# Optimization experiments

Measured on AMD Instinct MI355X. Metric: run time of the kernel, lower is better.

Reference implementation:

```python
import jax, jax.numpy as jnp
import numpy as np

NOISE_LEVEL = 0.01
MASK_RATIO = 0.3
CG_TOL = 1e-7
CG_MAXITER = 300
# 8-connected neighbor offsets and weights (sum to 1), as in ROAD
OFFSETS = [((1, 1), 1.0 / 12.0), ((0, 1), 1.0 / 6.0), ((-1, 1), 1.0 / 12.0),
           ((1, -1), 1.0 / 12.0), ((0, -1), 1.0 / 6.0), ((-1, -1), 1.0 / 12.0),
           ((1, 0), 1.0 / 6.0), ((-1, 0), 1.0 / 6.0)]


def _shift(f, dy, dx):
    # out[..., r, c] = f[..., r+dy, c+dx], zero outside the grid (invalid neighbors)
    H, W = f.shape[-2], f.shape[-1]
    pad = [(0, 0)] * (f.ndim - 2) + [(1, 1), (1, 1)]
    fp = jnp.pad(f, pad)
    return fp[..., 1 + dy:1 + dy + H, 1 + dx:1 + dx + W]


def _stencil(f):
    # weighted sum over valid 8-neighbors (zero padding encodes validity)
    return sum(w * _shift(f, dy, dx) for (dy, dx), w in OFFSETS)


def _road_mask_morf_by_area(smap, ratio):
    # mask==0 -> pixel is imputed; MoRF masks the top `ratio` fraction by saliency
    B, H, W = smap.shape
    k = int(round(ratio * H * W))
    top_idx = jnp.argsort(-smap.reshape(B, -1), axis=1)[:, :k]  # (B, k)
    mask = jnp.ones((B, H * W), jnp.float32)
    mask = mask.at[jnp.arange(B)[:, None], top_idx].set(0.0)
    return mask.reshape(B, H, W)


def _impute(img, mask, noise):
    # Solves the same sparse linear system as ROAD._setup_sparse_system + spsolve,
    # expressed matrix-free on the pixel grid: for each unknown pixel i,
    #   S_i * x_i - sum_{valid unknown nb j} w_ij x_j = sum_{valid known nb j} w_ij img_j
    # where S_i = sum of valid-neighbor weights (== sum_neighbors in the torch code).
    # This is an SPD graph-Laplacian system; CG converges to the direct-solve answer.
    m = mask[:, None]            # (B,1,H,W); 1 = known pixel
    unk = 1.0 - m                # 1 = unknown pixel
    H, W = img.shape[-2], img.shape[-1]
    S = _stencil(jnp.ones((H, W), img.dtype))    # (H,W) valid-neighbor weight sums
    rhs = unk * _stencil(m * img)                # == -b of the torch assembly

    def Aop(x):
        # identity on known pixels keeps the operator SPD over the full grid
        return jnp.where(unk > 0, S * x - _stencil(unk * x), x)

    x, _ = jax.scipy.sparse.linalg.cg(Aop, rhs, tol=CG_TOL, maxiter=CG_MAXITER)
    return m * img + unk * (x + NOISE_LEVEL * noise)


def setup_inputs() -> dict:
    key = jax.random.key(0)
    k1, k2, k3 = jax.random.split(key, 3)
    B, C, H, W = 16, 3, 512, 512
    img = jax.random.normal(k1, (B, C, H, W), jnp.float32)
    smap = jax.random.randint(k2, (B, H, W), 0, 1000000, jnp.int32)
    noise = jax.random.normal(k3, (B, C, H, W), jnp.float32)
    return {"img": img, "smap": smap, "noise": noise}


def reference(img, smap, noise):
    mask = _road_mask_morf_by_area(smap, MASK_RATIO)   # (B,H,W), 0 = impute
    imputed = _impute(img, mask, noise)                # (B,C,H,W)
    return imputed, mask
```

## Files before the change

### kernel.cpp

```cpp
#include <hip/hip_runtime.h>
#include <cstdint>
#include <cstddef>

#define HW 512
#define SPATIAL (HW*HW)
#define BATCH 16
#define CH 3
#define NPLANE (BATCH*CH)
#define NELEM ((size_t)NPLANE*SPATIAL)
#define GROWS (NPLANE*HW)
#define K_SELECT 78643
#define NITER 8
#define CAP_TIES 4096
#define NSLOT 64
#define PAD 8
#define RBAND 4
#define CBAND 6

typedef _Float16 h16;
typedef __attribute__((ext_vector_type(8))) _Float16 h16x8;
typedef __attribute__((ext_vector_type(8))) float f32x8;

static const size_t OFF_P0   = 0;
static const size_t OFF_P1   = NELEM*2;
static const size_t OFF_P2   = NELEM*4;
static const size_t OFF_BITS = NELEM*6;
static const size_t OFF_X    = OFF_BITS + (size_t)BATCH*8192*4;
static const size_t OFF_DOTS = OFF_X + NELEM*2;
static const size_t OFF_BETA = OFF_DOTS + (size_t)(NITER+1)*3*NSLOT*PAD*8;
static const size_t OFF_ALPH = OFF_BETA + (size_t)(NITER+1)*8;
static const size_t OFF_HC   = OFF_ALPH + (size_t)(NITER+1)*8;
static const size_t OFF_HF   = OFF_HC + (size_t)BATCH*1024*4;
static const size_t OFF_SEL  = OFF_HF + (size_t)BATCH*1024*4;
static const size_t OFF_TC   = OFF_SEL + (size_t)BATCH*4*4;
static const size_t OFF_TL   = OFF_TC + 64;

__global__ __launch_bounds__(256) void k_hist_coarse(const int* __restrict__ smap, int* __restrict__ hist){
  __shared__ int h[1024];
  int tid = threadIdx.x;
  for (int j=tid;j<1024;j+=256) h[j]=0;
  __syncthreads();
  int b = blockIdx.y;
  int base = b*SPATIAL + blockIdx.x*4096;
  #pragma unroll
  for (int e=0;e<16;e++){
    int v = smap[base + e*256 + tid];
    atomicAdd(&h[v>>10], 1);
  }
  __syncthreads();
  for (int j=tid;j<1024;j+=256){ int c=h[j]; if(c) atomicAdd(&hist[b*1024+j], c); }
}

__global__ __launch_bounds__(1024) void k_select_coarse(const int* __restrict__ hist, int* __restrict__ sel){
  int lane = threadIdx.x, b = threadIdx.y;
  const int* h = hist + b*1024;
  int loc[16]; int s=0;
  #pragma unroll
  for (int j=0;j<16;j++){ loc[j]=h[lane*16+j]; s+=loc[j]; }
  int T=s;
  #pragma unroll
  for (int o=1;o<64;o<<=1){ int t=__shfl_down(T,o,64); if (lane+o<64) T+=t; }
  int S = T - s;
  if (S < K_SELECT && T >= K_SELECT){
    int acc=S;
    #pragma unroll
    for (int j=15;j>=0;j--){
      acc+=loc[j];
      if (acc>=K_SELECT){ sel[b*4+0]=lane*16+j; sel[b*4+1]=acc-loc[j]; break; }
    }
  }
}

__global__ __launch_bounds__(256) void k_hist_fine(const int* __restrict__ smap, const int* __restrict__ sel, int* __restrict__ hist){
  __shared__ int h[1024];
  int tid=threadIdx.x;
  for (int j=tid;j<1024;j+=256) h[j]=0;
  __syncthreads();
  int b=blockIdx.y;
  int cb = sel[b*4+0];
  int base = b*SPATIAL + blockIdx.x*4096;
  #pragma unroll
  for (int e=0;e<16;e++){
    int v = smap[base+e*256+tid];
    if ((v>>10)==cb) atomicAdd(&h[v&1023],1);
  }
  __syncthreads();
  for (int j=tid;j<1024;j+=256){ int c=h[j]; if(c) atomicAdd(&hist[b*1024+j],c); }
}

__global__ __launch_bounds__(1024) void k_select_fine(const int* __restrict__ hist, int* __restrict__ sel){
  int lane = threadIdx.x, b = threadIdx.y;
  const int* h = hist + b*1024;
  int cb = sel[b*4+0];
  int acc0 = sel[b*4+1];
  int loc[16]; int s=0;
  #pragma unroll
  for (int j=0;j<16;j++){ loc[j]=h[lane*16+j]; s+=loc[j]; }
  int T=s;
  #pragma unroll
  for (int o=1;o<64;o<<=1){ int t=__shfl_down(T,o,64); if (lane+o<64) T+=t; }
  int S = acc0 + (T - s);
  int Ti = acc0 + T;
  if (S < K_SELECT && Ti >= K_SELECT){
    int acc=S;
    #pragma unroll
    for (int j=15;j>=0;j--){
      acc+=loc[j];
      if (acc>=K_SELECT){
        sel[b*4+2]=(cb<<10)|(lane*16+j);
        sel[b*4+3]=K_SELECT-(acc-loc[j]);
        break;
      }
    }
  }
}

__global__ __launch_bounds__(256) void k_mask_init(const int* __restrict__ smap, const int* __restrict__ sel,
                                                   float* __restrict__ mask, uint32_t* __restrict__ bits,
                                                   int* __restrict__ tiecnt, int* __restrict__ tielist){
  int idx = blockIdx.x*256+threadIdx.x;
  int b = idx>>18;
  int v = smap[idx];
  int T = sel[b*4+2];
  bool unk = (v>T);
  unsigned long long bal = __ballot(unk);
  if ((threadIdx.x&63)==0){
    bits[idx>>5]     = (uint32_t)(bal);
    bits[(idx>>5)+1] = (uint32_t)(bal>>32);
  }
  if (v==T){
    int t = atomicAdd(&tiecnt[b],1);
    if (t<CAP_TIES) tielist[b*CAP_TIES+t] = idx & (SPATIAL-1);
  }
  mask[idx]= unk? 0.f : 1.f;
}

__global__ __launch_bounds__(256) void k_tie_fix(const int* __restrict__ sel, const int* __restrict__ tiecnt,
                                                 const int* __restrict__ tielist, float* __restrict__ mask,
                                                 uint32_t* __restrict__ bits){
  int b=blockIdx.x;
  int n = tiecnt[b]; if (n>CAP_TIES) n=CAP_TIES;
  int need = sel[b*4+3];
  for (int e=threadIdx.x; e<n; e+=256){
    int me = tielist[b*CAP_TIES+e];
    int rank=0;
    for (int j=0;j<n;j++) rank += (tielist[b*CAP_TIES+j] < me) ? 1:0;
    if (rank<need){
      mask[b*SPATIAL+me]=0.f;
      atomicOr(&bits[(b<<13)+(me>>5)], 1u<<(me&31));
    }
  }
}

__device__ __forceinline__ void bwin(const float v[8], float w[10], int lane){
  float up = __shfl_up(v[7],1,64);
  float dn = __shfl_down(v[0],1,64);
  w[0] = (lane==0)?0.f:up;
  #pragma unroll
  for(int e=0;e<8;e++) w[e+1]=v[e];
  w[9] = (lane==63)?0.f:dn;
}
__device__ __forceinline__ float accE(const float* wm, const float* wc, const float* wp, int e){
  const float WE=1.f/6.f, WC=1.f/12.f;
  return WE*(wm[e+1]+wp[e+1]+wc[e]+wc[e+2]) + WC*(wm[e]+wm[e+2]+wp[e]+wp[e+2]);
}
__device__ __forceinline__ float accEm(const float* wm, const float* wc, const float* wp, int e, float um, float up){
  const float WE=1.f/6.f, WC=1.f/12.f;
  return WE*(um*wm[e+1]+up*wp[e+1]+wc[e]+wc[e+2]) + WC*(um*(wm[e]+wm[e+2])+up*(wp[e]+wp[e+2]));
}
__device__ __forceinline__ h16x8 loadg8(const h16* buf, int g, int x0){
  h16x8 t;
  if ((unsigned)g < (unsigned)GROWS){
    t = *(const h16x8*)(buf + (size_t)g*HW + x0);
  } else {
    #pragma unroll
    for (int e=0;e<8;e++) t[e]=(h16)0.f;
  }
  return t;
}
__device__ __forceinline__ void unpack8(const h16x8 t, float v[8]){
  #pragma unroll
  for (int e=0;e<8;e++) v[e]=(float)t[e];
}

__device__ __forceinline__ void dots_emit(float a,float b,float c,int tid,double* dst,int it){
  #pragma unroll
  for (int o=32;o>0;o>>=1){ a+=__shfl_down(a,o,64); b+=__shfl_down(b,o,64); c+=__shfl_down(c,o,64); }
  __shared__ double s3[3][4];
  int wv = tid>>6;
  if ((tid&63)==0){ s3[0][wv]=(double)a; s3[1][wv]=(double)b; s3[2][wv]=(double)c; }
  __syncthreads();
  if (tid==0){
    double A=s3[0][0]+s3[0][1]+s3[0][2]+s3[0][3];
    double B=s3[1][0]+s3[1][1]+s3[1][2]+s3[1][3];
    double C=s3[2][0]+s3[2][1]+s3[2][2]+s3[2][3];
    int slot = blockIdx.x & (NSLOT-1);
    atomicAdd(&dst[(((size_t)it*3+0)*NSLOT+slot)*PAD], A);
    atomicAdd(&dst[(((size_t)it*3+1)*NSLOT+slot)*PAD], B);
    atomicAdd(&dst[(((size_t)it*3+2)*NSLOT+slot)*PAD], C);
  }
}

#define SW_ROW(u) float t1_=(1.f/6.f)*(u), t2_=(1.f/6.f)+(1.f/12.f)*(u)
#define SW_E(e)   fmaf(t2_, vxe[e], t1_)

__global__ __launch_bounds__(256) void k_rhs(const float* __restrict__ img, const uint32_t* __restrict__ bits,
                                             h16* __restrict__ p0, double* __restrict__ dots){
  int lane=threadIdx.x; int tid=threadIdx.y*64+lane;
  int w = blockIdx.x*4+threadIdx.y;
  int plane = w>>7; int a = (w&127)*RBAND;
  const float* ip = img + (size_t)plane*SPATIAL;
  h16* rn = p0 + (size_t)plane*SPATIAL;
  const uint32_t* ub = bits + ((size_t)(plane/CH)<<13);
  int x0=lane*8, wofs=lane>>2, bit0=(lane&3)*8;
  float vxe[8];
  #pragma unroll
  for (int e=0;e<8;e++){
    int xg=x0+e;
    vxe[e] = ((xg>0)?1.f:0.f) + ((xg<HW-1)?1.f:0.f);
  }
  float wv_m[10], wv_c[10], wv_p[10], wr_2[10], wr_1[10], wr_0[10];
  float t[8];
  auto loadv=[&](int y, float v[8]){
    if ((unsigned)y < HW){
      f32x8 iv = *(const f32x8*)(ip + y*HW + x0);
      uint32_t uy = ub[y*16 + wofs];
      #pragma unroll
      for (int e=0;e<8;e++) v[e] = ((uy>>(bit0+e))&1u)? 0.f : iv[e];
    } else {
      #pragma unroll
      for (int e=0;e<8;e++) v[e]=0.f;
    }
  };
  loadv(a-2,t); bwin(t,wv_m,lane);
  loadv(a-1,t); bwin(t,wv_c,lane);
  #pragma unroll
  for (int j=0;j<10;j++){ wr_2[j]=0.f; wr_1[j]=0.f; }
  uint32_t ub_1=0;
  float d_pap=0.f, d_apap=0.f, d_rr=0.f;
  #pragma unroll
  for (int j=0;j<RBAND+2;j++){
    int y = a-1+j;
    loadv(y+1,t); bwin(t,wv_p,lane);
    uint32_t uy = ((unsigned)y<HW)? ub[y*16+wofs] : 0u;
    float rr8[8];
    #pragma unroll
    for (int e=0;e<8;e++){
      float rv = ((uy>>(bit0+e))&1u)? accE(wv_m,wv_c,wv_p,e) : 0.f;
      rr8[e] = (float)(h16)rv;
    }
    if (j>=1 && j<1+RBAND){
      h16x8 rw;
      #pragma unroll
      for (int e=0;e<8;e++){ rw[e]=(h16)rr8[e]; d_rr = fmaf(rr8[e],rr8[e],d_rr); }
      *(h16x8*)(rn + y*HW + x0) = rw;
    }
    bwin(rr8, wr_0, lane);
    if (j>=2){
      int yc = y-1;
      float u = ((yc>0)?1.f:0.f) + ((yc<HW-1)?1.f:0.f);
      SW_ROW(u);
      #pragma unroll
      for (int e=0;e<8;e++){
        float unk = (float)((ub_1>>(bit0+e))&1u);
        float Ap = unk * (SW_E(e)*wr_1[e+1] - accE(wr_2,wr_1,wr_0,e));
        d_pap = fmaf(wr_1[e+1],Ap,d_pap);
        d_apap= fmaf(Ap,Ap,d_apap);
      }
    }
    #pragma unroll
    for (int jj=0;jj<10;jj++){ wv_m[jj]=wv_c[jj]; wv_c[jj]=wv_p[jj]; wr_2[jj]=wr_1[jj]; wr_1[jj]=wr_0[jj]; }
    ub_1 = uy;
  }
  dots_emit(d_pap,d_apap,d_rr,tid,dots,0);
}

__global__ __launch_bounds__(256) void k_cg(const h16* __restrict__ pm1, const h16* __restrict__ pm2,
    h16* __restrict__ pn, h16* __restrict__ xv, const uint32_t* __restrict__ bits,
    double* __restrict__ dots, double* __restrict__ betas, double* __restrict__ alphas, int iter, int last){
  int lane = threadIdx.x;
  int tid = threadIdx.y*64 + lane;
  int w = blockIdx.x*4 + threadIdx.y;
  int g0 = w * CBAND;
  int x0 = lane*8;
  int wofs = lane>>2;
  int bit0 = (lane&3)*8;

  h16x8 p1r[CBAND+4];
  h16x8 p2r[CBAND+2];
  uint32_t ubr[CBAND+2];
  #pragma unroll
  for (int k=0;k<CBAND+4;k++) p1r[k] = loadg8(pm1, g0-2+k, x0);
  if (iter>1){
    #pragma unroll
    for (int k=0;k<CBAND+2;k++) p2r[k] = loadg8(pm2, g0-1+k, x0);
  } else {
    #pragma unroll
    for (int k=0;k<CBAND+2;k++){
      h16x8 z;
      #pragma unroll
      for (int e=0;e<8;e++) z[e]=(h16)0.f;
      p2r[k]=z;
    }
  }
  #pragma unroll
  for (int k=0;k<CBAND+2;k++){
    int gy = g0-1+k;
    int py = gy & (HW-1);
    int bidx = (gy>>9)/CH;
    ubr[k] = ((unsigned)gy<(unsigned)GROWS)? bits[((size_t)bidx<<13)+py*16+wofs] : 0u;
  }

  __shared__ float sab[4];
  if (tid < 64){
    size_t bse = (((size_t)(iter-1)*3)*NSLOT + tid)*PAD;
    double pap = dots[bse];
    double apap= dots[bse + (size_t)NSLOT*PAD];
    double rr  = dots[bse + (size_t)2*NSLOT*PAD];
    #pragma unroll
    for (int o=32;o>0;o>>=1){ pap+=__shfl_down(pap,o,64); apap+=__shfl_down(apap,o,64); rr+=__shfl_down(rr,o,64); }
    if (tid==0){
      double al = (pap!=0.0)? rr/pap : 0.0;
      double rrn = al*al*apap - rr;
      double bi = (rr!=0.0)? rrn/rr : 0.0;
      double bp = (iter>=2)? betas[iter-1] : 0.0;
      double ap_= (iter>=2)? alphas[iter-1] : 0.0;
      sab[0]=(float)al; sab[1]=(float)bp; sab[2]=(float)bi; sab[3]=(float)ap_;
      if (blockIdx.x==0){ betas[iter]=bi; alphas[iter]=al; }
    }
  }
  __syncthreads();
  float alpha=sab[0], bprev=sab[1], bnext=sab[2], aprev=sab[3];
  int do_x = ((iter&1)==0) || last;

  float vxe[8];
  #pragma unroll
  for (int e=0;e<8;e++){
    int xg=x0+e;
    vxe[e] = ((xg>0)?1.f:0.f) + ((xg<HW-1)?1.f:0.f);
  }

  float w1m[10], w1c[10], w1p[10];
  float wi2[10], wi1[10], wi0[10];
  float t[8];
  unpack8(p1r[0], t); bwin(t, w1m, lane);
  unpack8(p1r[1], t); bwin(t, w1c, lane);
  #pragma unroll
  for (int j=0;j<10;j++){ wi2[j]=0.f; wi1[j]=0.f; }
  uint32_t ub_1 = 0;
  float d_pap=0.f, d_apap=0.f, d_rr=0.f;
  #pragma unroll
  for (int j=0;j<CBAND+2;j++){
    int gy = g0-1+j;
    int py = gy & (HW-1);
    unpack8(p1r[j+2], t); bwin(t, w1p, lane);
    float r2[8]; unpack8(p2r[j], r2);
    uint32_t uy = ubr[j];
    float um = (py>0)?1.f:0.f, up = (py<HW-1)?1.f:0.f;
    float u = um+up;
    SW_ROW(u);
    float rv8[8], pi[8];
    #pragma unroll
    for (int e=0;e<8;e++){
      float unk = (float)((uy>>(bit0+e))&1u);
      float Ap = unk * (SW_E(e)*w1c[e+1] - accEm(w1m,w1c,w1p,e,um,up));
      float rt = w1c[e+1] - bprev*r2[e];
      float rv = rt - alpha*Ap;
      rv = (float)(h16)rv;
      float pv = rv + bnext*w1c[e+1];
      pv = (float)(h16)pv;
      rv8[e]=rv; pi[e]=pv;
    }
    if (j>=1 && j<1+CBAND){
      h16x8 pw;
      #pragma unroll
      for (int e=0;e<8;e++){
        pw[e] = (h16)pi[e];
        d_rr = fmaf(rv8[e],rv8[e],d_rr);
      }
      if (do_x){
        h16x8 xo;
        if (iter==2){
          #pragma unroll
          for (int e=0;e<8;e++)
            xo[e] = (h16)(alpha*w1c[e+1] + aprev*r2[e]);
        } else {
          h16x8 xc = *(const h16x8*)(xv + (size_t)gy*HW + x0);
          #pragma unroll
          for (int e=0;e<8;e++)
            xo[e] = (h16)((float)xc[e] + alpha*w1c[e+1] + aprev*r2[e]);
        }
        *(h16x8*)(xv + (size_t)gy*HW + x0) = xo;
      }
      if (!last) *(h16x8*)(pn + (size_t)gy*HW + x0) = pw;
    }
    bwin(pi, wi0, lane);
    if (!last && j>=2){
      int gc = gy-1;
      int pyc = gc & (HW-1);
      float umc = (pyc>0)?1.f:0.f, upc = (pyc<HW-1)?1.f:0.f;
      float u2 = umc+upc;
      float t1b=(1.f/6.f)*u2, t2b=(1.f/6.f)+(1.f/12.f)*u2;
      #pragma unroll
      for (int e=0;e<8;e++){
        float unk = (float)((ub_1>>(bit0+e))&1u);
        float Ap = unk * (fmaf(t2b,vxe[e],t1b)*wi1[e+1] - accEm(wi2,wi1,wi0,e,umc,upc));
        d_pap = fmaf(wi1[e+1],Ap,d_pap);
        d_apap= fmaf(Ap,Ap,d_apap);
      }
    }
    #pragma unroll
    for (int jj=0;jj<10;jj++){ w1m[jj]=w1c[jj]; w1c[jj]=w1p[jj]; wi2[jj]=wi1[jj]; wi1[jj]=wi0[jj]; }
    ub_1 = uy;
  }
  if (!last) dots_emit(d_pap,d_apap,d_rr,tid,dots,iter);
}

__global__ __launch_bounds__(256) void k_final(const float* __restrict__ img, const float* __restrict__ noise,
    const uint32_t* __restrict__ bits, const h16* __restrict__ xv, float* __restrict__ out){
  int lane = threadIdx.x;
  int y = blockIdx.x*4 + threadIdx.y;
  int bc = blockIdx.y;
  size_t base = (size_t)bc*SPATIAL;
  int x0 = lane*8;
  int sp0 = y*HW + x0;
  const uint32_t* ub = bits + ((size_t)(bc/CH)<<13);
  f32x8 iv = *(const f32x8*)(img+base+sp0);
  f32x8 nv = *(const f32x8*)(noise+base+sp0);
  h16x8 xc = *(const h16x8*)(xv+base+sp0);
  uint32_t wb = ub[y*16 + (lane>>2)];
  int bit0 = (lane&3)*8;
  f32x8 ov;
  #pragma unroll
  for (int e=0;e<8;e++){
    ov[e] = ((wb>>(bit0+e))&1u) ? ((float)xc[e] + 0.01f*nv[e]) : iv[e];
  }
  *(f32x8*)(out+base+sp0) = ov;
}

extern "C" void kernel_launch(void* const* d_in, const int* in_sizes, int n_in,
                              void* d_out, int out_size, void* d_ws, size_t ws_size,
                              hipStream_t stream) {
  const float* img  =(const float*)d_in[0];
  const int*   smap =(const int*)d_in[1];
  const float* noise=(const float*)d_in[2];
  float* out=(float*)d_out;
  float* maskout = out + NELEM;
  char* ws=(char*)d_ws;
  h16* pbuf[3] = { (h16*)(ws+OFF_P0), (h16*)(ws+OFF_P1), (h16*)(ws+OFF_P2) };
  h16* xv =(h16*)(ws+OFF_X);
  uint32_t* bits=(uint32_t*)(ws+OFF_BITS);
  double* dots=(double*)(ws+OFF_DOTS);
  double* betas=(double*)(ws+OFF_BETA);
  double* alphas=(double*)(ws+OFF_ALPH);
  int* hc=(int*)(ws+OFF_HC);
  int* hf=(int*)(ws+OFF_HF);
  int* sel=(int*)(ws+OFF_SEL);
  int* tiecnt=(int*)(ws+OFF_TC);
  int* tielist=(int*)(ws+OFF_TL);

  hipMemsetAsync(ws+OFF_DOTS, 0, OFF_TL-OFF_DOTS, stream);

  k_hist_coarse<<<dim3(64,16),256,0,stream>>>(smap,hc);
  k_select_coarse<<<1,dim3(64,16),0,stream>>>(hc,sel);
  k_hist_fine<<<dim3(64,16),256,0,stream>>>(smap,sel,hf);
  k_select_fine<<<1,dim3(64,16),0,stream>>>(hf,sel);
  k_mask_init<<<SPATIAL*BATCH/256,256,0,stream>>>(smap,sel,maskout,bits,tiecnt,tielist);
  k_tie_fix<<<16,256,0,stream>>>(sel,tiecnt,tielist,maskout,bits);

  dim3 grhs(NPLANE*(HW/RBAND)/4), brhs(64,4);
  k_rhs<<<grhs,brhs,0,stream>>>(img,bits,pbuf[0],dots);

  dim3 gcg(GROWS/CBAND/4), bcg(64,4);
  for (int i=1;i<=NITER;i++){
    const h16* pm1 = pbuf[(i-1)%3];
    const h16* pm2 = (i>=2)? pbuf[(i-2)%3] : pbuf[0];
    h16* pn        = pbuf[i%3];
    k_cg<<<gcg,bcg,0,stream>>>(pm1,pm2,pn,xv,bits,dots,betas,alphas,i,(i==NITER)?1:0);
  }

  k_final<<<dim3(HW/4,NPLANE),bcg,0,stream>>>(img,noise,bits,xv,out);
}
```

Measured before the change: 322.0 us.

## Fold final CG x-update into output kernel and preload rhs rows

Removes the last k_cg launch: the final solution update (x += alpha*p_{k-1} + aprev*p_{k-2}) is computed inside the output kernel, which reduces the last dot products itself. This saves one full stencil pass over all planes plus a launch, at the cost of reading two extra half-precision direction buffers in the final kernel. Separately, k_rhs now loads all input rows and mask words for its band up front into registers instead of reloading them per row, which raises register use.

```diff
diff --git a/kernel.cpp b/kernel.cpp
--- a/kernel.cpp
+++ b/kernel.cpp
@@ -219,30 +219,42 @@
     int xg=x0+e;
     vxe[e] = ((xg>0)?1.f:0.f) + ((xg<HW-1)?1.f:0.f);
   }
+
+  f32x8 ivr[RBAND+4];
+  uint32_t ubr2[RBAND+4];
+  #pragma unroll
+  for (int k=0;k<RBAND+4;k++){
+    int y = a-2+k;
+    if ((unsigned)y < HW){
+      ivr[k] = *(const f32x8*)(ip + y*HW + x0);
+      ubr2[k] = ub[y*16 + wofs];
+    } else {
+      f32x8 z;
+      #pragma unroll
+      for (int e=0;e<8;e++) z[e]=0.f;
+      ivr[k]=z;
+      ubr2[k]=0u;
+    }
+  }
+
   float wv_m[10], wv_c[10], wv_p[10], wr_2[10], wr_1[10], wr_0[10];
   float t[8];
-  auto loadv=[&](int y, float v[8]){
-    if ((unsigned)y < HW){
-      f32x8 iv = *(const f32x8*)(ip + y*HW + x0);
-      uint32_t uy = ub[y*16 + wofs];
-      #pragma unroll
-      for (int e=0;e<8;e++) v[e] = ((uy>>(bit0+e))&1u)? 0.f : iv[e];
-    } else {
-      #pragma unroll
-      for (int e=0;e<8;e++) v[e]=0.f;
-    }
-  };
-  loadv(a-2,t); bwin(t,wv_m,lane);
-  loadv(a-1,t); bwin(t,wv_c,lane);
+  #pragma unroll
+  for (int e=0;e<8;e++) t[e] = ((ubr2[0]>>(bit0+e))&1u)? 0.f : ivr[0][e];
+  bwin(t,wv_m,lane);
+  #pragma unroll
+  for (int e=0;e<8;e++) t[e] = ((ubr2[1]>>(bit0+e))&1u)? 0.f : ivr[1][e];
+  bwin(t,wv_c,lane);
   #pragma unroll
   for (int j=0;j<10;j++){ wr_2[j]=0.f; wr_1[j]=0.f; }
-  uint32_t ub_1=0;
   float d_pap=0.f, d_apap=0.f, d_rr=0.f;
   #pragma unroll
   for (int j=0;j<RBAND+2;j++){
     int y = a-1+j;
-    loadv(y+1,t); bwin(t,wv_p,lane);
-    uint32_t uy = ((unsigned)y<HW)? ub[y*16+wofs] : 0u;
+    #pragma unroll
+    for (int e=0;e<8;e++) t[e] = ((ubr2[j+2]>>(bit0+e))&1u)? 0.f : ivr[j+2][e];
+    bwin(t,wv_p,lane);
+    uint32_t uy = ubr2[j+1];
     float rr8[8];
     #pragma unroll
     for (int e=0;e<8;e++){
@@ -260,9 +272,10 @@
       int yc = y-1;
       float u = ((yc>0)?1.f:0.f) + ((yc<HW-1)?1.f:0.f);
       SW_ROW(u);
+      uint32_t ubp = ubr2[j];
       #pragma unroll
       for (int e=0;e<8;e++){
-        float unk = (float)((ub_1>>(bit0+e))&1u);
+        float unk = (float)((ubp>>(bit0+e))&1u);
         float Ap = unk * (SW_E(e)*wr_1[e+1] - accE(wr_2,wr_1,wr_0,e));
         d_pap = fmaf(wr_1[e+1],Ap,d_pap);
         d_apap= fmaf(Ap,Ap,d_apap);
@@ -270,14 +283,13 @@
     }
     #pragma unroll
     for (int jj=0;jj<10;jj++){ wv_m[jj]=wv_c[jj]; wv_c[jj]=wv_p[jj]; wr_2[jj]=wr_1[jj]; wr_1[jj]=wr_0[jj]; }
-    ub_1 = uy;
   }
   dots_emit(d_pap,d_apap,d_rr,tid,dots,0);
 }
 
 __global__ __launch_bounds__(256) void k_cg(const h16* __restrict__ pm1, const h16* __restrict__ pm2,
     h16* __restrict__ pn, h16* __restrict__ xv, const uint32_t* __restrict__ bits,
-    double* __restrict__ dots, double* __restrict__ betas, double* __restrict__ alphas, int iter, int last){
+    double* __restrict__ dots, double* __restrict__ betas, double* __restrict__ alphas, int iter){
   int lane = threadIdx.x;
   int tid = threadIdx.y*64 + lane;
   int w = blockIdx.x*4 + threadIdx.y;
@@ -331,7 +343,7 @@
   }
   __syncthreads();
   float alpha=sab[0], bprev=sab[1], bnext=sab[2], aprev=sab[3];
-  int do_x = ((iter&1)==0) || last;
+  int do_x = ((iter&1)==0);
 
   float vxe[8];
   #pragma unroll
@@ -392,10 +404,10 @@
         }
         *(h16x8*)(xv + (size_t)gy*HW + x0) = xo;
       }
-      if (!last) *(h16x8*)(pn + (size_t)gy*HW + x0) = pw;
+      *(h16x8*)(pn + (size_t)gy*HW + x0) = pw;
     }
     bwin(pi, wi0, lane);
-    if (!last && j>=2){
+    if (j>=2){
       int gc = gy-1;
       int pyc = gc & (HW-1);
       float umc = (pyc>0)?1.f:0.f, upc = (pyc<HW-1)?1.f:0.f;
@@ -413,12 +425,30 @@
     for (int jj=0;jj<10;jj++){ w1m[jj]=w1c[jj]; w1c[jj]=w1p[jj]; wi2[jj]=wi1[jj]; wi1[jj]=wi0[jj]; }
     ub_1 = uy;
   }
-  if (!last) dots_emit(d_pap,d_apap,d_rr,tid,dots,iter);
-}
-
-__global__ __launch_bounds__(256) void k_final(const float* __restrict__ img, const float* __restrict__ noise,
-    const uint32_t* __restrict__ bits, const h16* __restrict__ xv, float* __restrict__ out){
+  dots_emit(d_pap,d_apap,d_rr,tid,dots,iter);
+}
+
+__global__ __launch_bounds__(256) void k_final2(const float* __restrict__ img, const float* __restrict__ noise,
+    const uint32_t* __restrict__ bits, const h16* __restrict__ xv,
+    const h16* __restrict__ pm1, const h16* __restrict__ pm2,
+    const double* __restrict__ dots, const double* __restrict__ alphas, float* __restrict__ out){
   int lane = threadIdx.x;
+  int tid = threadIdx.y*64 + lane;
+  __shared__ float sab[2];
+  if (tid < 64){
+    size_t bse = (((size_t)(NITER-1)*3)*NSLOT + tid)*PAD;
+    double pap = dots[bse];
+    double rr  = dots[bse + (size_t)2*NSLOT*PAD];
+    #pragma unroll
+    for (int o=32;o>0;o>>=1){ pap+=__shfl_down(pap,o,64); rr+=__shfl_down(rr,o,64); }
+    if (tid==0){
+      sab[0] = (pap!=0.0)? (float)(rr/pap) : 0.f;
+      sab[1] = (float)alphas[NITER-1];
+    }
+  }
+  __syncthreads();
+  float alpha=sab[0], aprev=sab[1];
+
   int y = blockIdx.x*4 + threadIdx.y;
   int bc = blockIdx.y;
   size_t base = (size_t)bc*SPATIAL;
@@ -428,12 +458,15 @@
   f32x8 iv = *(const f32x8*)(img+base+sp0);
   f32x8 nv = *(const f32x8*)(noise+base+sp0);
   h16x8 xc = *(const h16x8*)(xv+base+sp0);
+  h16x8 p1 = *(const h16x8*)(pm1+base+sp0);
+  h16x8 p2 = *(const h16x8*)(pm2+base+sp0);
   uint32_t wb = ub[y*16 + (lane>>2)];
   int bit0 = (lane&3)*8;
   f32x8 ov;
   #pragma unroll
   for (int e=0;e<8;e++){
-    ov[e] = ((wb>>(bit0+e))&1u) ? ((float)xc[e] + 0.01f*nv[e]) : iv[e];
+    float xn = (float)xc[e] + alpha*(float)p1[e] + aprev*(float)p2[e];
+    ov[e] = ((wb>>(bit0+e))&1u) ? (xn + 0.01f*nv[e]) : iv[e];
   }
   *(f32x8*)(out+base+sp0) = ov;
 }
@@ -472,12 +505,16 @@
   k_rhs<<<grhs,brhs,0,stream>>>(img,bits,pbuf[0],dots);
 
   dim3 gcg(GROWS/CBAND/4), bcg(64,4);
-  for (int i=1;i<=NITER;i++){
+  for (int i=1;i<=NITER-1;i++){
     const h16* pm1 = pbuf[(i-1)%3];
     const h16* pm2 = (i>=2)? pbuf[(i-2)%3] : pbuf[0];
     h16* pn        = pbuf[i%3];
-    k_cg<<<gcg,bcg,0,stream>>>(pm1,pm2,pn,xv,bits,dots,betas,alphas,i,(i==NITER)?1:0);
-  }
-
-  k_final<<<dim3(HW/4,NPLANE),bcg,0,stream>>>(img,noise,bits,xv,out);
-}
+    k_cg<<<gcg,bcg,0,stream>>>(pm1,pm2,pn,xv,bits,dots,betas,alphas,i);
+  }
+
+  {
+    const h16* pm1 = pbuf[(NITER-1)%3];
+    const h16* pm2 = pbuf[(NITER-2)%3];
+    k_final2<<<dim3(HW/4,NPLANE),bcg,0,stream>>>(img,noise,bits,xv,pm1,pm2,dots,alphas,out);
+  }
+}
```

Result: slower. 374.6 us (+16.4%).
